# Performance work log

Hardware: AMD Instinct MI355X
Metric: run time of the kernel (lower is better)

Reference implementation:

```python
import jax, jax.numpy as jnp
import numpy as np
import math

D_MODEL = 1024
NUM_HEADS = 16
HEAD_DIM = D_MODEL // NUM_HEADS
B, T = 2, 2048


def _linear_params(key, d_in, d_out):
    kw, kb = jax.random.split(key)
    s = 1.0 / math.sqrt(d_in)
    W = jax.random.uniform(kw, (d_in, d_out), jnp.float32, -s, s)
    b = jax.random.uniform(kb, (d_out,), jnp.float32, -s, s)
    return W, b


def setup_inputs() -> dict:
    key = jax.random.key(0)
    ks = jax.random.split(key, 10)
    x_real = jax.random.normal(ks[0], (B, T, D_MODEL), jnp.float32)
    x_imag = jax.random.normal(ks[1], (B, T, D_MODEL), jnp.float32)
    Wqr, bqr = _linear_params(ks[2], D_MODEL, D_MODEL)
    Wqi, bqi = _linear_params(ks[3], D_MODEL, D_MODEL)
    Wkr, bkr = _linear_params(ks[4], D_MODEL, D_MODEL)
    Wki, bki = _linear_params(ks[5], D_MODEL, D_MODEL)
    Wvr, bvr = _linear_params(ks[6], D_MODEL, D_MODEL)
    Wvi, bvi = _linear_params(ks[7], D_MODEL, D_MODEL)
    Wor, bor = _linear_params(ks[8], D_MODEL, D_MODEL)
    Woi, boi = _linear_params(ks[9], D_MODEL, D_MODEL)
    return dict(x_real=x_real, x_imag=x_imag,
                Wqr=Wqr, bqr=bqr, Wqi=Wqi, bqi=bqi,
                Wkr=Wkr, bkr=bkr, Wki=Wki, bki=bki,
                Wvr=Wvr, bvr=bvr, Wvi=Wvi, bvi=bvi,
                Wor=Wor, bor=bor, Woi=Woi, boi=boi)


def _heads(x):
    # (B,T,C) -> (B,H,T,Dh)
    b, t, _ = x.shape
    return x.reshape(b, t, NUM_HEADS, HEAD_DIM).transpose(0, 2, 1, 3)


def reference(x_real, x_imag,
              Wqr, bqr, Wqi, bqi, Wkr, bkr, Wki, bki,
              Wvr, bvr, Wvi, bvi, Wor, bor, Woi, boi):
    b, t, c = x_real.shape
    # NOTE: first two qr/qi assignments in the torch forward are dead code;
    # effective math is below.
    qr = _heads(x_real @ Wqr + bqr)
    qi = _heads(x_imag @ Wqi + bqi)
    kr = _heads(x_real @ Wkr + bkr)
    ki = _heads(x_imag @ Wki + bki)
    vr = _heads(x_real @ Wvr + bvr)
    vi = _heads(x_imag @ Wvi + bvi)
    # Re(Q K^H) score: Qr*Kr + Qi*Ki, scaled
    score = (jnp.einsum('bhtd,bhsd->bhts', qr, kr)
             + jnp.einsum('bhtd,bhsd->bhts', qi, ki)) / math.sqrt(HEAD_DIM)
    causal = jnp.triu(jnp.ones((t, t), dtype=bool), k=1)  # True above diagonal
    score = jnp.where(causal[None, None], -jnp.inf, score)
    attn = jax.nn.softmax(score, axis=-1)
    out_r = jnp.einsum('bhts,bhsd->bhtd', attn, vr).transpose(0, 2, 1, 3).reshape(b, t, c)
    out_i = jnp.einsum('bhts,bhsd->bhtd', attn, vi).transpose(0, 2, 1, 3).reshape(b, t, c)
    final_r = out_r @ Wor + bor
    final_i = out_i @ Woi + boi
    return (final_r, final_i)
```

## Files before the change

kernel.cpp:

```cpp
#include <hip/hip_runtime.h>
#include <hip/hip_bf16.h>


typedef __attribute__((ext_vector_type(8))) __bf16 bf16x8;
typedef __attribute__((ext_vector_type(4))) float f32x4;
typedef __attribute__((ext_vector_type(16))) float f32x16;
typedef unsigned short u16;
typedef unsigned int u32;

#define L2E 1.44269504088896340736f
#define NEG16L2E (-23.0831207542234f)

__device__ __forceinline__ void gl2lds16(const void* g, void* l) {
  __builtin_amdgcn_global_load_lds(
      (const __attribute__((address_space(1))) unsigned int*)g,
      (__attribute__((address_space(3))) unsigned int*)l, 16, 0, 0);
}

__device__ __forceinline__ u16 f2bf(float f) {
  union { float f; unsigned u; } v;
  v.f = f;
  unsigned r = v.u + 0x7FFFu + ((v.u >> 16) & 1u);
  return (u16)(r >> 16);
}

__device__ __forceinline__ u32 cvtpk(float lo, float hi) {
  u32 d;
  asm("v_cvt_pk_bf16_f32 %0, %1, %2" : "=v"(d) : "v"(lo), "v"(hi));
  return d;
}

__global__ void cvt_bf16_2(const float* __restrict__ a, const float* __restrict__ bsrc,
                           u16* __restrict__ oa, u16* __restrict__ ob, int n) {
  const float* in = blockIdx.y ? bsrc : a;
  u16* out = blockIdx.y ? ob : oa;
  int stride = gridDim.x * blockDim.x * 4;
  for (int i = (blockIdx.x * blockDim.x + threadIdx.x) * 4; i < n; i += stride) {
    float4 v = *(const float4*)(in + i);
    ushort4 o;
    o.x = f2bf(v.x); o.y = f2bf(v.y); o.z = f2bf(v.z); o.w = f2bf(v.w);
    *(ushort4*)(out + i) = o;
  }
}

struct WPtrs { const float* w[8]; };

__global__ void cvt_w_t(WPtrs ptrs, u16* __restrict__ out) {
  __shared__ float tile[32][33];
  const float* W = ptrs.w[blockIdx.z];
  u16* o = out + ((size_t)blockIdx.z << 20);
  int tx = threadIdx.x & 31, ty = threadIdx.x >> 5;
  int bx = blockIdx.x * 32, by = blockIdx.y * 32;
#pragma unroll
  for (int k = 0; k < 4; k++) {
    int r = by + ty + k * 8;
    tile[ty + k * 8][tx] = W[(size_t)r * 1024 + bx + tx];
  }
  __syncthreads();
#pragma unroll
  for (int k = 0; k < 4; k++) {
    int n = bx + ty + k * 8;
    o[(size_t)n * 1024 + by + tx] = f2bf(tile[tx][ty + k * 8]);
  }
}

struct GemmArgs {
  const u16* A[6];
  const u16* Wt[6];
  const float* bias[6];
  void* dst[6];
  int off[6];
  int vt[6];
  float scale[6];
};

template <int MODE>
__global__ __launch_bounds__(256, 2) void gemm_bf16(GemmArgs args) {
  extern __shared__ u16 dynpad[];
  const int z = blockIdx.z;
  const u16* __restrict__ A = args.A[z];
  const u16* __restrict__ Bt = args.Wt[z];
  const float* __restrict__ bias = args.bias[z];
  const int brow = blockIdx.x * 128;
  const int bcol = blockIdx.y * 128;

  __shared__ u16 smem[2][2][128 * 32];

  const int tid = threadIdx.x;
  const int w = tid >> 6, lane = tid & 63;
  const int ql = lane & 15, hi = lane >> 4;
  const int wrow = (w >> 1) * 64, wcol = (w & 1) * 64;

  if (args.off[z] == -12345) ((volatile u16*)dynpad)[0] = 0;

  f32x4 acc[4][4] = {};

  auto stage = [&](int buf, int t) {
    int k0 = t * 32;
#pragma unroll
    for (int s = 0; s < 2; s++) {
      int q = w * 2 + s;
      int lr = q * 16 + (lane >> 2);
      int csrc = (lane & 3) ^ ((lr >> 1) & 3);
      gl2lds16(A + (size_t)(brow + lr) * 1024 + k0 + csrc * 8, &smem[0][buf][q * 512]);
    }
#pragma unroll
    for (int s = 0; s < 2; s++) {
      int q = w * 2 + s;
      int lr = q * 16 + (lane >> 2);
      int csrc = (lane & 3) ^ ((lr >> 1) & 3);
      gl2lds16(Bt + (size_t)(bcol + lr) * 1024 + k0 + csrc * 8, &smem[1][buf][q * 512]);
    }
  };

  stage(0, 0);
  __syncthreads();

  int buf = 0;
  for (int t = 0; t < 32; t++) {
    if (t + 1 < 32) stage(buf ^ 1, t + 1);
    bf16x8 a[4], b[4];
#pragma unroll
    for (int i = 0; i < 4; i++) {
      int row = wrow + i * 16 + ql;
      int cs = hi ^ ((row >> 1) & 3);
      a[i] = *(const bf16x8*)&smem[0][buf][row * 32 + cs * 8];
      int col = wcol + i * 16 + ql;
      int cs2 = hi ^ ((col >> 1) & 3);
      b[i] = *(const bf16x8*)&smem[1][buf][col * 32 + cs2 * 8];
    }
#pragma unroll
    for (int i = 0; i < 4; i++)
#pragma unroll
      for (int j = 0; j < 4; j++)
        acc[i][j] = __builtin_amdgcn_mfma_f32_16x16x32_bf16(a[i], b[j], acc[i][j], 0, 0, 0);
    __syncthreads();
    buf ^= 1;
  }

  const int off = args.off[z];
  const float scl = args.scale[z];

  if (MODE == 1 && args.vt[z]) {
    u16* sm = &smem[0][0][0];
    const int bb = brow >> 11, t0 = brow & 2047;
    const int h0 = bcol >> 6;
    u16* dstV = (u16*)args.dst[z];
#pragma unroll
    for (int p = 0; p < 2; p++) {
      if ((w & 1) == p) {
#pragma unroll
        for (int i = 0; i < 4; i++)
#pragma unroll
          for (int j = 0; j < 4; j++) {
            int col_local = j * 16 + ql;
            int row_base = wrow + i * 16 + hi * 4;
            float bv = bias[bcol + p * 64 + col_local];
            union { __bf16 hh[4]; uint2 u; } cv;
#pragma unroll
            for (int r = 0; r < 4; r++) cv.hh[r] = (__bf16)((acc[i][j][r] + bv) * scl);
            *(uint2*)&sm[col_local * 136 + row_base] = cv.u;
          }
      }
      __syncthreads();
      {
        int dh = tid >> 2, tq = tid & 3;
        const u16* src = &sm[dh * 136 + tq * 32];
        u16* dp = dstV + ((size_t)((bb * 16 + h0 + p) * 128) + off + dh) * 2048 + t0 + tq * 32;
#pragma unroll
        for (int k = 0; k < 4; k++)
          *(uint4*)(dp + k * 8) = *(const uint4*)(src + k * 8);
      }
      __syncthreads();
    }
    return;
  }

#pragma unroll
  for (int i = 0; i < 4; i++)
#pragma unroll
    for (int j = 0; j < 4; j++)
#pragma unroll
      for (int r = 0; r < 4; r++) {
        int grow = brow + wrow + i * 16 + hi * 4 + r;
        int gcol = bcol + wcol + j * 16 + ql;
        float v = (acc[i][j][r] + bias[gcol]) * scl;
        if (MODE == 0) {
          ((float*)args.dst[z])[(size_t)grow * 1024 + gcol] = v;
        } else {
          int bb = grow >> 11, tt = grow & 2047;
          int h = gcol >> 6, dh = gcol & 63;
          ((u16*)args.dst[z])[(((size_t)(bb * 16 + h) * 2048 + tt) << 7) + off + dh] = f2bf(v);
        }
      }
}

__global__ __launch_bounds__(256, 3) void attn_kernel(
    const u16* __restrict__ Q, const u16* __restrict__ K, const u16* __restrict__ Vt,
    u16* __restrict__ Or, u16* __restrict__ Oi) {
  const int bh = blockIdx.x;
  const int ii = (int)gridDim.y - 1 - (int)blockIdx.y;
  const int tid = threadIdx.x, w = tid >> 6, lane = tid & 63;
  const int q32 = lane & 31;
  const int hb = lane >> 5;
  const int wq = w & 1, wk = w >> 1;
  const int b = bh >> 4, hh = bh & 15;

  __shared__ u16 lK[64 * 128];
  __shared__ u16 lV[128 * 64];
  __shared__ u16 lP[4][32 * 32];

  const int q = ii * 64 + wq * 32 + q32;

  bf16x8 qf[8];
#pragma unroll
  for (int kk = 0; kk < 8; kk++)
    qf[kk] = *(const bf16x8*)(Q + ((size_t)bh * 2048 + q) * 128 + kk * 16 + hb * 8);

  f32x16 o[4] = {};
  float l = 0.f;

  const int nt = ii + 1;

  auto stageKV = [&](int jt) {
#pragma unroll
    for (int s = 0; s < 4; s++) {
      int op = w * 4 + s;
      int srow = op * 4 + (lane >> 4);
      int csrc = (lane & 15) ^ (srow & 15);
      gl2lds16(K + ((size_t)bh * 2048 + jt * 64 + srow) * 128 + csrc * 8, &lK[op * 512]);
    }
#pragma unroll
    for (int s = 0; s < 4; s++) {
      int op = w * 4 + s;
      int dv = op * 8 + (lane >> 3);
      int csrc = (lane & 7) ^ (dv & 7);
      gl2lds16(Vt + ((size_t)bh * 128 + dv) * 2048 + jt * 64 + csrc * 8, &lV[op * 512]);
    }
  };

  for (int jt = 0; jt < nt; jt++) {
    stageKV(jt);
    asm volatile("s_waitcnt vmcnt(0)" ::: "memory");
    __syncthreads();

    if (jt * 64 + wk * 32 <= ii * 64 + wq * 32 + 31) {
      f32x16 s = {};
      __builtin_amdgcn_s_setprio(1);
#pragma unroll
      for (int kk = 0; kk < 8; kk++) {
        int ch = kk * 2 + hb;
        int r = wk * 32 + q32;
        bf16x8 kf = *(const bf16x8*)&lK[r * 128 + (ch ^ (r & 15)) * 8];
        s = __builtin_amdgcn_mfma_f32_32x32x16_bf16(kf, qf[kk], s, 0, 0, 0);
      }
      __builtin_amdgcn_s_setprio(0);

      if (jt * 64 + wk * 32 + 31 > ii * 64 + wq * 32) {
#pragma unroll
        for (int reg = 0; reg < 16; reg++) {
          int krow = (reg & 3) + 8 * (reg >> 2) + 4 * hb;
          int kg = jt * 64 + wk * 32 + krow;
          if (kg > q) s[reg] = -1e30f;
        }
      }

#pragma unroll
      for (int rq = 0; rq < 4; rq++) {
        float p0 = exp2f(__builtin_fmaf(s[rq * 4 + 0], L2E, NEG16L2E));
        float p1 = exp2f(__builtin_fmaf(s[rq * 4 + 1], L2E, NEG16L2E));
        float p2 = exp2f(__builtin_fmaf(s[rq * 4 + 2], L2E, NEG16L2E));
        float p3 = exp2f(__builtin_fmaf(s[rq * 4 + 3], L2E, NEG16L2E));
        l += (p0 + p1) + (p2 + p3);
        int byte_off = q32 * 64 + ((rq ^ (q32 & 3)) * 16) + hb * 8;
        uint2 pk2;
        pk2.x = cvtpk(p0, p1);
        pk2.y = cvtpk(p2, p3);
        *(uint2*)((char*)&lP[w][0] + byte_off) = pk2;
      }
      asm volatile("s_waitcnt lgkmcnt(0)" ::: "memory");
      __builtin_amdgcn_sched_barrier(0);

      __builtin_amdgcn_s_setprio(1);
#pragma unroll
      for (int kk2 = 0; kk2 < 2; kk2++) {
        int G = kk2 * 2 + hb;
        bf16x8 pf = *(const bf16x8*)((char*)&lP[w][0] + q32 * 64 + ((G ^ (q32 & 3)) * 16));
#pragma unroll
        for (int jv2 = 0; jv2 < 4; jv2++) {
          int dv = jv2 * 32 + q32;
          int ch = wk * 4 + kk2 * 2 + hb;
          bf16x8 vf = *(const bf16x8*)&lV[dv * 64 + (ch ^ (dv & 7)) * 8];
          o[jv2] = __builtin_amdgcn_mfma_f32_32x32x16_bf16(vf, pf, o[jv2], 0, 0, 0);
        }
      }
      __builtin_amdgcn_s_setprio(0);
    }

    __syncthreads();
  }

  l += __shfl_xor(l, 32);
  float* mL = (float*)&lP[0][0];

  if (w >= 2) {
    float* mO = (w == 2) ? (float*)&lK[0] : (float*)&lV[0];
#pragma unroll
    for (int jv2 = 0; jv2 < 4; jv2++)
#pragma unroll
      for (int rq = 0; rq < 4; rq++) {
        int dvb = jv2 * 32 + rq * 8 + 4 * hb;
        int dvs = (dvb + 4 * q32) & 127;
        f32x4 t;
        t[0] = o[jv2][rq * 4 + 0]; t[1] = o[jv2][rq * 4 + 1];
        t[2] = o[jv2][rq * 4 + 2]; t[3] = o[jv2][rq * 4 + 3];
        *(f32x4*)&mO[q32 * 128 + dvs] = t;
      }
    if (lane < 32) mL[(w - 2) * 32 + q32] = l;
  }
  __syncthreads();

  if (w < 2) {
    float* mO = (w == 0) ? (float*)&lK[0] : (float*)&lV[0];
    float lt = l + mL[w * 32 + q32];
    float linv = 1.f / lt;
    const size_t obase = ((size_t)b * 2048 + q) * 1024 + hh * 64;
#pragma unroll
    for (int jv2 = 0; jv2 < 4; jv2++)
#pragma unroll
      for (int rq = 0; rq < 4; rq++) {
        int dvb = jv2 * 32 + rq * 8 + 4 * hb;
        int dvs = (dvb + 4 * q32) & 127;
        f32x4 part = *(const f32x4*)&mO[q32 * 128 + dvs];
        union { __bf16 hh4[4]; ushort4 u; } cv;
#pragma unroll
        for (int r = 0; r < 4; r++)
          cv.hh4[r] = (__bf16)((o[jv2][rq * 4 + r] + part[r]) * linv);
        u16* dst = (jv2 < 2) ? Or : Oi;
        *(ushort4*)(dst + obase + (jv2 & 1) * 32 + rq * 8 + 4 * hb) = cv.u;
      }
  }
}

extern "C" void kernel_launch(void* const* d_in, const int* in_sizes, int n_in,
                              void* d_out, int out_size, void* d_ws, size_t ws_size,
                              hipStream_t stream) {
  (void)in_sizes; (void)n_in; (void)out_size; (void)ws_size;

  const float* x_real = (const float*)d_in[0];
  const float* x_imag = (const float*)d_in[1];

  char* ws = (char*)d_ws;
  size_t off = 0;
  auto alloc = [&](size_t bytes) {
    void* p = ws + off;
    off += (bytes + 255) & ~(size_t)255;
    return p;
  };
  const size_t MK = 4096ull * 1024;
  u16* xr16 = (u16*)alloc(MK * 2);
  u16* xi16 = (u16*)alloc(MK * 2);
  u16* Wt   = (u16*)alloc(8ull * 1024 * 1024 * 2);
  u16* Qc   = (u16*)alloc(32ull * 2048 * 128 * 2);
  u16* Kc   = (u16*)alloc(32ull * 2048 * 128 * 2);
  u16* Vt   = (u16*)alloc(32ull * 2048 * 128 * 2);
  u16* Or   = (u16*)alloc(MK * 2);
  u16* Oi   = (u16*)alloc(MK * 2);

  cvt_bf16_2<<<dim3(1024, 2), 256, 0, stream>>>(x_real, x_imag, xr16, xi16, (int)MK);

  WPtrs wp;
  wp.w[0] = (const float*)d_in[2];
  wp.w[1] = (const float*)d_in[4];
  wp.w[2] = (const float*)d_in[6];
  wp.w[3] = (const float*)d_in[8];
  wp.w[4] = (const float*)d_in[10];
  wp.w[5] = (const float*)d_in[12];
  wp.w[6] = (const float*)d_in[14];
  wp.w[7] = (const float*)d_in[16];
  cvt_w_t<<<dim3(32, 32, 8), 256, 0, stream>>>(wp, Wt);

  GemmArgs pa{};
  const u16* xs[2] = {xr16, xi16};
  for (int z = 0; z < 6; z++) {
    pa.A[z] = xs[z & 1];
    pa.Wt[z] = Wt + (size_t)z * 1048576;
    pa.off[z] = (z & 1) * 64;
    pa.vt[z] = (z >= 4) ? 1 : 0;
    pa.scale[z] = (z < 2) ? 0.125f : 1.0f;
  }
  pa.bias[0] = (const float*)d_in[3];
  pa.bias[1] = (const float*)d_in[5];
  pa.bias[2] = (const float*)d_in[7];
  pa.bias[3] = (const float*)d_in[9];
  pa.bias[4] = (const float*)d_in[11];
  pa.bias[5] = (const float*)d_in[13];
  pa.dst[0] = Qc; pa.dst[1] = Qc;
  pa.dst[2] = Kc; pa.dst[3] = Kc;
  pa.dst[4] = Vt; pa.dst[5] = Vt;
  gemm_bf16<1><<<dim3(32, 8, 6), 256, 16384, stream>>>(pa);

  attn_kernel<<<dim3(32, 32), 256, 0, stream>>>(Qc, Kc, Vt, Or, Oi);

  GemmArgs fa{};
  fa.A[0] = Or; fa.A[1] = Oi;
  fa.Wt[0] = Wt + 6ull * 1048576;
  fa.Wt[1] = Wt + 7ull * 1048576;
  fa.bias[0] = (const float*)d_in[15];
  fa.bias[1] = (const float*)d_in[17];
  fa.dst[0] = (float*)d_out;
  fa.dst[1] = (float*)d_out + MK;
  fa.off[0] = 0; fa.off[1] = 0;
  fa.vt[0] = 0; fa.vt[1] = 0;
  fa.scale[0] = 1.0f; fa.scale[1] = 1.0f;
  gemm_bf16<0><<<dim3(32, 8, 2), 256, 16384, stream>>>(fa);
}
```

Before: 181.6 us.

## Stage 128-key tiles and have each wave process both query halves

The attention kernel now stages 128 keys of K and V per iteration instead of 64. Each of the four waves owns a 32-key window and computes scores and PV products for all 64 queries (two 32-query sets), so each K and V fragment read from LDS is reused across two MFMAs. This halves the number of loop iterations and barriers. It replaces the old two-way split-K merge with a four-way LDS reduction across waves, done in two passes for the real and imaginary outputs. In exchange it doubles LDS use (64KB+16KB), raises register pressure, and lowers launch bounds occupancy from 3 to 2 blocks. It also wastes more work on the causal diagonal, since a 128-key tile can overshoot a 64-query block.

```diff
diff --git a/kernel.cpp b/kernel.cpp
--- a/kernel.cpp
+++ b/kernel.cpp
@@ -195,7 +195,7 @@
       }
 }
 
-__global__ __launch_bounds__(256, 3) void attn_kernel(
+__global__ __launch_bounds__(256, 2) void attn_kernel(
     const u16* __restrict__ Q, const u16* __restrict__ K, const u16* __restrict__ Vt,
     u16* __restrict__ Or, u16* __restrict__ Oi) {
   const int bh = blockIdx.x;
@@ -203,80 +203,95 @@
   const int tid = threadIdx.x, w = tid >> 6, lane = tid & 63;
   const int q32 = lane & 31;
   const int hb = lane >> 5;
-  const int wq = w & 1, wk = w >> 1;
   const int b = bh >> 4, hh = bh & 15;
 
-  __shared__ u16 lK[64 * 128];
-  __shared__ u16 lV[128 * 64];
-  __shared__ u16 lP[4][32 * 32];
-
-  const int q = ii * 64 + wq * 32 + q32;
-
-  bf16x8 qf[8];
-#pragma unroll
-  for (int kk = 0; kk < 8; kk++)
-    qf[kk] = *(const bf16x8*)(Q + ((size_t)bh * 2048 + q) * 128 + kk * 16 + hb * 8);
-
-  f32x16 o[4] = {};
-  float l = 0.f;
-
-  const int nt = ii + 1;
+  __shared__ u16 lKV[2][128 * 128];
+  __shared__ u16 lP[8][1024];
+  u16* lK = lKV[0];
+  u16* lV = lKV[1];
+
+  const int qA = ii * 64 + q32;
+  const int qB = qA + 32;
+  const int kwin = w * 32;
+
+  bf16x8 qfA[8], qfB[8];
+#pragma unroll
+  for (int kk = 0; kk < 8; kk++) {
+    qfA[kk] = *(const bf16x8*)(Q + ((size_t)bh * 2048 + qA) * 128 + kk * 16 + hb * 8);
+    qfB[kk] = *(const bf16x8*)(Q + ((size_t)bh * 2048 + qB) * 128 + kk * 16 + hb * 8);
+  }
+
+  f32x16 oA[4] = {}, oB[4] = {};
+  float lA = 0.f, lB = 0.f;
+
+  const int nt2 = (ii + 2) >> 1;
 
   auto stageKV = [&](int jt) {
 #pragma unroll
-    for (int s = 0; s < 4; s++) {
-      int op = w * 4 + s;
+    for (int s = 0; s < 8; s++) {
+      int op = w * 8 + s;
       int srow = op * 4 + (lane >> 4);
       int csrc = (lane & 15) ^ (srow & 15);
-      gl2lds16(K + ((size_t)bh * 2048 + jt * 64 + srow) * 128 + csrc * 8, &lK[op * 512]);
-    }
-#pragma unroll
-    for (int s = 0; s < 4; s++) {
-      int op = w * 4 + s;
-      int dv = op * 8 + (lane >> 3);
-      int csrc = (lane & 7) ^ (dv & 7);
-      gl2lds16(Vt + ((size_t)bh * 128 + dv) * 2048 + jt * 64 + csrc * 8, &lV[op * 512]);
+      gl2lds16(K + ((size_t)bh * 2048 + jt * 128 + srow) * 128 + csrc * 8, &lK[op * 512]);
+    }
+#pragma unroll
+    for (int s = 0; s < 8; s++) {
+      int op = w * 8 + s;
+      int dv = op * 4 + (lane >> 4);
+      int csrc = (lane & 15) ^ (dv & 15);
+      gl2lds16(Vt + ((size_t)bh * 128 + dv) * 2048 + jt * 128 + csrc * 8, &lV[op * 512]);
     }
   };
 
-  for (int jt = 0; jt < nt; jt++) {
+  for (int jt = 0; jt < nt2; jt++) {
     stageKV(jt);
     asm volatile("s_waitcnt vmcnt(0)" ::: "memory");
     __syncthreads();
 
-    if (jt * 64 + wk * 32 <= ii * 64 + wq * 32 + 31) {
-      f32x16 s = {};
+    if (jt * 128 + kwin <= ii * 64 + 63) {
+      f32x16 sA = {}, sB = {};
       __builtin_amdgcn_s_setprio(1);
 #pragma unroll
       for (int kk = 0; kk < 8; kk++) {
         int ch = kk * 2 + hb;
-        int r = wk * 32 + q32;
-        bf16x8 kf = *(const bf16x8*)&lK[r * 128 + (ch ^ (r & 15)) * 8];
-        s = __builtin_amdgcn_mfma_f32_32x32x16_bf16(kf, qf[kk], s, 0, 0, 0);
+        int r = kwin + q32;
+        bf16x8 kf = *(const bf16x8*)&lK[r * 128 + ((ch ^ (r & 15)) * 8)];
+        sA = __builtin_amdgcn_mfma_f32_32x32x16_bf16(kf, qfA[kk], sA, 0, 0, 0);
+        sB = __builtin_amdgcn_mfma_f32_32x32x16_bf16(kf, qfB[kk], sB, 0, 0, 0);
       }
       __builtin_amdgcn_s_setprio(0);
 
-      if (jt * 64 + wk * 32 + 31 > ii * 64 + wq * 32) {
+      if (jt * 128 + kwin + 31 > ii * 64) {
 #pragma unroll
         for (int reg = 0; reg < 16; reg++) {
           int krow = (reg & 3) + 8 * (reg >> 2) + 4 * hb;
-          int kg = jt * 64 + wk * 32 + krow;
-          if (kg > q) s[reg] = -1e30f;
+          int kg = jt * 128 + kwin + krow;
+          if (kg > qA) sA[reg] = -1e30f;
+          if (kg > qB) sB[reg] = -1e30f;
         }
       }
 
 #pragma unroll
       for (int rq = 0; rq < 4; rq++) {
-        float p0 = exp2f(__builtin_fmaf(s[rq * 4 + 0], L2E, NEG16L2E));
-        float p1 = exp2f(__builtin_fmaf(s[rq * 4 + 1], L2E, NEG16L2E));
-        float p2 = exp2f(__builtin_fmaf(s[rq * 4 + 2], L2E, NEG16L2E));
-        float p3 = exp2f(__builtin_fmaf(s[rq * 4 + 3], L2E, NEG16L2E));
-        l += (p0 + p1) + (p2 + p3);
+        float a0 = exp2f(__builtin_fmaf(sA[rq * 4 + 0], L2E, NEG16L2E));
+        float a1 = exp2f(__builtin_fmaf(sA[rq * 4 + 1], L2E, NEG16L2E));
+        float a2 = exp2f(__builtin_fmaf(sA[rq * 4 + 2], L2E, NEG16L2E));
+        float a3 = exp2f(__builtin_fmaf(sA[rq * 4 + 3], L2E, NEG16L2E));
+        lA += (a0 + a1) + (a2 + a3);
         int byte_off = q32 * 64 + ((rq ^ (q32 & 3)) * 16) + hb * 8;
         uint2 pk2;
-        pk2.x = cvtpk(p0, p1);
-        pk2.y = cvtpk(p2, p3);
-        *(uint2*)((char*)&lP[w][0] + byte_off) = pk2;
+        pk2.x = cvtpk(a0, a1);
+        pk2.y = cvtpk(a2, a3);
+        *(uint2*)((char*)&lP[w * 2][0] + byte_off) = pk2;
+
+        float b0 = exp2f(__builtin_fmaf(sB[rq * 4 + 0], L2E, NEG16L2E));
+        float b1 = exp2f(__builtin_fmaf(sB[rq * 4 + 1], L2E, NEG16L2E));
+        float b2 = exp2f(__builtin_fmaf(sB[rq * 4 + 2], L2E, NEG16L2E));
+        float b3 = exp2f(__builtin_fmaf(sB[rq * 4 + 3], L2E, NEG16L2E));
+        lB += (b0 + b1) + (b2 + b3);
+        pk2.x = cvtpk(b0, b1);
+        pk2.y = cvtpk(b2, b3);
+        *(uint2*)((char*)&lP[w * 2 + 1][0] + byte_off) = pk2;
       }
       asm volatile("s_waitcnt lgkmcnt(0)" ::: "memory");
       __builtin_amdgcn_sched_barrier(0);
@@ -285,13 +300,16 @@
 #pragma unroll
       for (int kk2 = 0; kk2 < 2; kk2++) {
         int G = kk2 * 2 + hb;
-        bf16x8 pf = *(const bf16x8*)((char*)&lP[w][0] + q32 * 64 + ((G ^ (q32 & 3)) * 16));
+        int pb = q32 * 64 + ((G ^ (q32 & 3)) * 16);
+        bf16x8 pfA = *(const bf16x8*)((char*)&lP[w * 2][0] + pb);
+        bf16x8 pfB = *(const bf16x8*)((char*)&lP[w * 2 + 1][0] + pb);
 #pragma unroll
         for (int jv2 = 0; jv2 < 4; jv2++) {
           int dv = jv2 * 32 + q32;
-          int ch = wk * 4 + kk2 * 2 + hb;
-          bf16x8 vf = *(const bf16x8*)&lV[dv * 64 + (ch ^ (dv & 7)) * 8];
-          o[jv2] = __builtin_amdgcn_mfma_f32_32x32x16_bf16(vf, pf, o[jv2], 0, 0, 0);
+          int g = w * 4 + kk2 * 2 + hb;
+          bf16x8 vf = *(const bf16x8*)&lV[dv * 128 + ((g ^ (dv & 15)) * 8)];
+          oA[jv2] = __builtin_amdgcn_mfma_f32_32x32x16_bf16(vf, pfA, oA[jv2], 0, 0, 0);
+          oB[jv2] = __builtin_amdgcn_mfma_f32_32x32x16_bf16(vf, pfB, oB[jv2], 0, 0, 0);
         }
       }
       __builtin_amdgcn_s_setprio(0);
@@ -300,45 +318,65 @@
     __syncthreads();
   }
 
-  l += __shfl_xor(l, 32);
+  lA += __shfl_xor(lA, 32);
+  lB += __shfl_xor(lB, 32);
   float* mL = (float*)&lP[0][0];
-
-  if (w >= 2) {
-    float* mO = (w == 2) ? (float*)&lK[0] : (float*)&lV[0];
-#pragma unroll
-    for (int jv2 = 0; jv2 < 4; jv2++)
-#pragma unroll
-      for (int rq = 0; rq < 4; rq++) {
-        int dvb = jv2 * 32 + rq * 8 + 4 * hb;
-        int dvs = (dvb + 4 * q32) & 127;
-        f32x4 t;
-        t[0] = o[jv2][rq * 4 + 0]; t[1] = o[jv2][rq * 4 + 1];
-        t[2] = o[jv2][rq * 4 + 2]; t[3] = o[jv2][rq * 4 + 3];
-        *(f32x4*)&mO[q32 * 128 + dvs] = t;
-      }
-    if (lane < 32) mL[(w - 2) * 32 + q32] = l;
-  }
-  __syncthreads();
-
-  if (w < 2) {
-    float* mO = (w == 0) ? (float*)&lK[0] : (float*)&lV[0];
-    float lt = l + mL[w * 32 + q32];
-    float linv = 1.f / lt;
-    const size_t obase = ((size_t)b * 2048 + q) * 1024 + hh * 64;
-#pragma unroll
-    for (int jv2 = 0; jv2 < 4; jv2++)
-#pragma unroll
-      for (int rq = 0; rq < 4; rq++) {
-        int dvb = jv2 * 32 + rq * 8 + 4 * hb;
-        int dvs = (dvb + 4 * q32) & 127;
-        f32x4 part = *(const f32x4*)&mO[q32 * 128 + dvs];
-        union { __bf16 hh4[4]; ushort4 u; } cv;
-#pragma unroll
-        for (int r = 0; r < 4; r++)
-          cv.hh4[r] = (__bf16)((o[jv2][rq * 4 + r] + part[r]) * linv);
-        u16* dst = (jv2 < 2) ? Or : Oi;
-        *(ushort4*)(dst + obase + (jv2 & 1) * 32 + rq * 8 + 4 * hb) = cv.u;
-      }
+  float* mrg = (float*)&lKV[0][0];
+
+  if (lane < 32) {
+    mL[w * 64 + q32] = lA;
+    mL[w * 64 + 32 + q32] = lB;
+  }
+
+  float linv = 0.f;
+#pragma unroll
+  for (int r = 0; r < 2; r++) {
+#pragma unroll
+    for (int set = 0; set < 2; set++) {
+      int qcol = set * 32 + q32;
+#pragma unroll
+      for (int jl = 0; jl < 2; jl++) {
+        int jv2 = r * 2 + jl;
+#pragma unroll
+        for (int rq = 0; rq < 4; rq++) {
+          int dvb = jl * 32 + rq * 8 + 4 * hb;
+          int dvs = (dvb + 4 * qcol) & 63;
+          f32x4 t;
+          if (set == 0) {
+            t[0] = oA[jv2][rq * 4 + 0]; t[1] = oA[jv2][rq * 4 + 1];
+            t[2] = oA[jv2][rq * 4 + 2]; t[3] = oA[jv2][rq * 4 + 3];
+          } else {
+            t[0] = oB[jv2][rq * 4 + 0]; t[1] = oB[jv2][rq * 4 + 1];
+            t[2] = oB[jv2][rq * 4 + 2]; t[3] = oB[jv2][rq * 4 + 3];
+          }
+          *(f32x4*)&mrg[w * 4096 + qcol * 64 + dvs] = t;
+        }
+      }
+    }
+    __syncthreads();
+
+    int qr = w * 16 + (lane >> 2);
+    if (r == 0) {
+      float lt = mL[qr] + mL[64 + qr] + mL[128 + qr] + mL[192 + qr];
+      linv = 1.f / lt;
+    }
+    u16* dst = (r == 0) ? Or : Oi;
+    const size_t obase = ((size_t)b * 2048 + ii * 64 + qr) * 1024 + hh * 64 + (lane & 3) * 16;
+#pragma unroll
+    for (int c = 0; c < 4; c++) {
+      int dv4 = (lane & 3) * 16 + c * 4;
+      int dvs = (dv4 + 4 * qr) & 63;
+      f32x4 s0 = *(const f32x4*)&mrg[0 * 4096 + qr * 64 + dvs];
+      f32x4 s1 = *(const f32x4*)&mrg[1 * 4096 + qr * 64 + dvs];
+      f32x4 s2 = *(const f32x4*)&mrg[2 * 4096 + qr * 64 + dvs];
+      f32x4 s3 = *(const f32x4*)&mrg[3 * 4096 + qr * 64 + dvs];
+      f32x4 sum = (s0 + s1) + (s2 + s3);
+      union { __bf16 hh4[4]; ushort4 u; } cv;
+#pragma unroll
+      for (int j = 0; j < 4; j++) cv.hh4[j] = (__bf16)(sum[j] * linv);
+      *(ushort4*)(dst + obase + c * 4) = cv.u;
+    }
+    if (r == 0) __syncthreads();
   }
 }
 
```

Result: slower. 241.2 us (+32.8%).
